# Kernel tuning notes

Measured on AMD Instinct MI355X. Metric: run time of the kernel, lower is better.

Reference implementation:

```python
import jax, jax.numpy as jnp
import numpy as np

VOCAB = 32000
EMBED = 256
HIDDEN = 512
BATCH = 64
SEQ = 512


def setup_inputs() -> dict:
    key = jax.random.key(0)
    k1, k2, k3, k4, k5, k6 = jax.random.split(key, 6)
    s = 1.0 / np.sqrt(HIDDEN)
    return {
        "source": jax.random.randint(k1, (BATCH, SEQ), 0, VOCAB),
        "embedding": jax.random.normal(k2, (VOCAB, EMBED), dtype=jnp.float32),
        "W_ih": jax.random.uniform(k3, (EMBED, HIDDEN), dtype=jnp.float32, minval=-s, maxval=s),
        "W_hh": jax.random.uniform(k4, (HIDDEN, HIDDEN), dtype=jnp.float32, minval=-s, maxval=s),
        "b_ih": jax.random.uniform(k5, (HIDDEN,), dtype=jnp.float32, minval=-s, maxval=s),
        "b_hh": jax.random.uniform(k6, (HIDDEN,), dtype=jnp.float32, minval=-s, maxval=s),
    }


def reference(source, embedding, W_ih, W_hh, b_ih, b_hh):
    # Embedding lookup: (B, S, E)
    embedded = embedding[source]
    batch_size = source.shape[0]
    h0 = jnp.zeros((batch_size, HIDDEN), dtype=embedding.dtype)

    def step(h, x_t):
        # Elman RNN cell: h' = tanh(x W_ih + b_ih + h W_hh + b_hh)
        h_new = jnp.tanh(x_t @ W_ih + b_ih + h @ W_hh + b_hh)
        return h_new, h_new

    # scan over time axis: xs shape (S, B, E)
    _, hiddens = jax.lax.scan(step, h0, jnp.swapaxes(embedded, 0, 1))
    # hiddens: (S, B, H) -> (B, S, H)
    return jnp.swapaxes(hiddens, 0, 1)
```

## Files before the change

### kernel.cpp

```cpp
#include <hip/hip_runtime.h>
#include <stdint.h>

#define EMBED  256
#define HIDDEN 512
#define BATCH  64
#define SEQ    512

typedef _Float16 f16x8 __attribute__((ext_vector_type(8)));
typedef _Float16 f16x4 __attribute__((ext_vector_type(4)));
typedef float    f32x4 __attribute__((ext_vector_type(4)));


#define WIH_FRAGS (8 * 32 * 64 * 8)
#define WHH_FRAGS (16 * 32 * 64 * 8)

__global__ void prep_pack(const float* __restrict__ W_ih,
                          const float* __restrict__ W_hh,
                          unsigned short* __restrict__ wih_p,
                          unsigned short* __restrict__ whh_p) {
    int tid = blockIdx.x * blockDim.x + threadIdx.x;
    if (tid < WIH_FRAGS) {
        int j = tid & 7, l = (tid >> 3) & 63, nt = (tid >> 9) & 31, s = tid >> 14;
        int k   = s * 32 + ((l >> 4) << 3) + j;
        int col = (nt << 4) + (l & 15);
        wih_p[tid] = __builtin_bit_cast(unsigned short, (_Float16)W_ih[k * HIDDEN + col]);
    } else {
        int t2 = tid - WIH_FRAGS;
        if (t2 < WHH_FRAGS) {
            int j = t2 & 7, l = (t2 >> 3) & 63, mt = (t2 >> 9) & 31, s = t2 >> 14;
            int k   = s * 32 + ((l >> 4) << 3) + j;
            int col = (mt << 4) + (l & 15);
            whh_p[t2] = __builtin_bit_cast(unsigned short, (_Float16)W_hh[k * HIDDEN + col]);
        }
    }
}

__global__ __launch_bounds__(256) void enc_gemm_ih(
    const int* __restrict__ source,
    const float* __restrict__ embedding,
    const unsigned short* __restrict__ wih_p,
    const float* __restrict__ b_ih,
    const float* __restrict__ b_hh,
    float* __restrict__ out)
{
    const int lane = threadIdx.x & 63;
    const int mt   = (blockIdx.x << 2) + (threadIdx.x >> 6);
    const int r0   = mt << 4;
    const int g    = lane >> 4;
    const int c    = lane & 15;

    const int idx = source[r0 + c];
    const float* erow = embedding + (size_t)idx * EMBED;

    f16x8 afrag[8];
#pragma unroll
    for (int s = 0; s < 8; ++s) {
        const float* p = erow + (s << 5) + (g << 3);
        f32x4 f0 = *(const f32x4*)p;
        f32x4 f1 = *(const f32x4*)(p + 4);
        f16x8 a;
        a[0] = (_Float16)f0[0]; a[1] = (_Float16)f0[1];
        a[2] = (_Float16)f0[2]; a[3] = (_Float16)f0[3];
        a[4] = (_Float16)f1[0]; a[5] = (_Float16)f1[1];
        a[6] = (_Float16)f1[2]; a[7] = (_Float16)f1[3];
        afrag[s] = a;
    }

    const f16x8* wp = (const f16x8*)wih_p;
    for (int nt = 0; nt < 32; ++nt) {
        f32x4 acc = {0.f, 0.f, 0.f, 0.f};
#pragma unroll
        for (int s = 0; s < 8; ++s) {
            f16x8 bfr = wp[(((s << 5) + nt) << 6) + lane];
            acc = __builtin_amdgcn_mfma_f32_16x16x32_f16(afrag[s], bfr, acc, 0, 0, 0);
        }
        const int col  = (nt << 4) + c;
        const float bias = b_ih[col] + b_hh[col];
        char* ob = (char*)out + (size_t)(r0 + (g << 2)) * 2048 + 1024 + (col << 1);
#pragma unroll
        for (int r = 0; r < 4; ++r)
            *(_Float16*)(ob + (size_t)r * 2048) = (_Float16)(acc[r] + bias);
    }
}

__global__ __launch_bounds__(512, 1) void enc_rnn(
    const unsigned short* __restrict__ whh_p,
    float* __restrict__ out)
{
    extern __shared__ char lds[];
    char* hbase = lds;
    char* wbase = lds + 32768;

    const int tid  = threadIdx.x;
    const int lane = tid & 63;
    const int w    = tid >> 6;
    const int g    = lane >> 4;
    const int c    = lane & 15;
    const int cx   = c & 7;
    const int mt0  = w << 2;

    const f16x8* wp = (const f16x8*)whh_p;

    {
        char* wl0 = wbase + ((w * 12) << 10) + (lane << 4);
#pragma unroll
        for (int fid = 0; fid < 12; ++fid) {
            int s = 9 + (fid >> 2), m = fid & 3;
            *(f16x8*)(wl0 + (fid << 10)) = wp[((s * 32 + mt0 + m) << 6) + lane];
        }
    }
    for (int i = tid; i < 32768 / 4; i += 512) ((int*)hbase)[i] = 0;

    f16x8 wreg[36];
#pragma unroll
    for (int s = 0; s < 9; ++s)
#pragma unroll
        for (int m = 0; m < 4; ++m)
            wreg[s * 4 + m] = wp[((s * 32 + mt0 + m) << 6) + lane];
#pragma unroll
    for (int i = 0; i < 36; ++i)
        asm volatile("" : "+v"(wreg[i]));

    __syncthreads();

    const int ch = cx >> 2;
    char* hb2 = hbase + (c << 10) + ((g ^ (cx & 3)) << 4);
    char* hev = hb2 + (ch << 6);
    char* hod = hb2 - (ch << 6);
    char* hw[4];
#pragma unroll
    for (int m = 0; m < 4; ++m) {
        int u = (w << 3) | ((m ^ (cx >> 1)) << 1) | ((g >> 1) ^ (cx & 1));
        hw[m] = hbase + (c << 10) + (u << 4) + ((g & 1) << 3);
    }
    char* ga = (char*)out + (size_t)((blockIdx.x << 4) + c) * SEQ * 2048
             + (w << 7) + (g << 3);
    const char* sp12 = (const char*)whh_p + ((12 * 32 + mt0) << 10) + (lane << 4);
    const char* sp13 = (const char*)whh_p + ((13 * 32 + mt0) << 10) + (lane << 4);
    const char* sp14 = (const char*)whh_p + ((14 * 32 + mt0) << 10) + (lane << 4);
    const char* sp15 = (const char*)whh_p + ((15 * 32 + mt0) << 10) + (lane << 4);
    char* wl = wbase + ((w * 12) << 10) + (lane << 4);

    auto STEP = [&](int RB, int RBN, int TB) {
        f16x8 sA[4], sB[4], sC[4];
#pragma unroll
        for (int m = 0; m < 4; ++m) sA[m] = *(const f16x8*)(sp12 + (m << 10));
#pragma unroll
        for (int m = 0; m < 4; ++m) sB[m] = *(const f16x8*)(sp13 + (m << 10));
        f16x4 pre[4];
#pragma unroll
        for (int m = 0; m < 4; ++m)
            pre[m] = *(const f16x4*)(ga + TB + 1024 + (m << 5));

        f32x4 acc[4];
#pragma unroll
        for (int m = 0; m < 4; ++m) acc[m] = (f32x4){0.f, 0.f, 0.f, 0.f};

#pragma unroll
        for (int s = 0; s < 16; ++s) {
            f16x8 h = *(const f16x8*)(((s & 1) ? hod : hev) + (s << 6) + RB);
            if (s == 6) {
#pragma unroll
                for (int m = 0; m < 4; ++m) sC[m] = *(const f16x8*)(sp14 + (m << 10));
            }
#pragma unroll
            for (int m = 0; m < 4; ++m) {
                f16x8 wv;
                if (s < 9)        wv = wreg[s * 4 + m];
                else if (s < 12)  wv = *(const f16x8*)(wl + ((((s - 9) << 2) | m) << 10));
                else if (s == 12) wv = sA[m];
                else if (s == 13) wv = sB[m];
                else if (s == 14) wv = sC[m];
                else              wv = sA[m];
                acc[m] = __builtin_amdgcn_mfma_f32_16x16x32_f16(wv, h, acc[m], 0, 0, 0);
            }
            if (s == 12) {
#pragma unroll
                for (int m = 0; m < 4; ++m) sA[m] = *(const f16x8*)(sp15 + (m << 10));
            }
        }

#pragma unroll
        for (int m = 0; m < 4; ++m) {
            f16x4 hv;
#pragma unroll
            for (int r = 0; r < 4; ++r) {
                float x  = acc[m][r] + (float)pre[m][r];
                float e  = __expf(2.0f * x);
                hv[r] = (_Float16)(1.0f - 2.0f * __builtin_amdgcn_rcpf(e + 1.0f));
            }
            *(f16x4*)(ga + TB + (m << 5)) = hv;
            *(f16x4*)(hw[m] + RBN) = hv;
        }
        __syncthreads();
    };

#pragma unroll 1
    for (int tp = 0; tp < SEQ; tp += 2) {
        STEP(0, 16384, 0);
        STEP(16384, 0, 2048);
        ga += 4096;
    }
}

__global__ __launch_bounds__(256) void expand_rows(float* __restrict__ out) {
    const int lane = threadIdx.x & 63;
    const int row  = (blockIdx.x << 2) + (threadIdx.x >> 6);
    char* rp = (char*)out + ((size_t)row << 11);
    f16x8 v = *(const f16x8*)(rp + (lane << 4));
    f32x4 lo, hi;
#pragma unroll
    for (int i = 0; i < 4; ++i) { lo[i] = (float)v[i]; hi[i] = (float)v[i + 4]; }
    *(f32x4*)(rp + (lane << 5))      = lo;
    *(f32x4*)(rp + (lane << 5) + 16) = hi;
}

extern "C" void kernel_launch(void* const* d_in, const int* in_sizes, int n_in,
                              void* d_out, int out_size, void* d_ws, size_t ws_size,
                              hipStream_t stream) {
    const int*   source    = (const int*)d_in[0];
    const float* embedding = (const float*)d_in[1];
    const float* W_ih      = (const float*)d_in[2];
    const float* W_hh      = (const float*)d_in[3];
    const float* b_ih      = (const float*)d_in[4];
    const float* b_hh      = (const float*)d_in[5];
    float* out = (float*)d_out;

    unsigned short* wih_p = (unsigned short*)d_ws;
    unsigned short* whh_p = wih_p + WIH_FRAGS;

    prep_pack<<<(WIH_FRAGS + WHH_FRAGS) / 256, 256, 0, stream>>>(W_ih, W_hh, wih_p, whh_p);
    enc_gemm_ih<<<512, 256, 0, stream>>>(source, embedding, wih_p, b_ih, b_hh, out);
    enc_rnn<<<4, 512, 131072, stream>>>(whh_p, out);
    expand_rows<<<8192, 256, 0, stream>>>(out);
}
```

Before: 1.299 ms.

## Hold 11 W_hh k-slices in registers via inline-asm MFMA chain in RNN step

Grows the register-resident part of W_hh from 9 to 11 k-slices. The first 11 MFMA groups are issued from one inline-asm block so the compiler cannot spill or reorder those weight registers. LDS-staged slices shift to 11-13, and only slices 14-15 are still streamed from global memory each step, down from four. Register pressure goes up sharply with 44 f16x8 weight registers plus 11 h fragments, and the min-blocks hint in launch_bounds is dropped, so spills or lost latency hiding are possible.

```diff
diff --git a/kernel.cpp b/kernel.cpp
--- a/kernel.cpp
+++ b/kernel.cpp
@@ -83,7 +83,15 @@
     }
 }
 
-__global__ __launch_bounds__(512, 1) void enc_rnn(
+#define MM(s) \
+  "v_mfma_f32_16x16x32_f16 %[a0], %[w" #s "0], %[h" #s "], %[a0]\n\t" \
+  "v_mfma_f32_16x16x32_f16 %[a1], %[w" #s "1], %[h" #s "], %[a1]\n\t" \
+  "v_mfma_f32_16x16x32_f16 %[a2], %[w" #s "2], %[h" #s "], %[a2]\n\t" \
+  "v_mfma_f32_16x16x32_f16 %[a3], %[w" #s "3], %[h" #s "], %[a3]\n\t"
+#define WOPS(s) [w##s##0]"v"(wv[4*s+0]), [w##s##1]"v"(wv[4*s+1]), \
+                [w##s##2]"v"(wv[4*s+2]), [w##s##3]"v"(wv[4*s+3])
+
+__global__ __launch_bounds__(512) void enc_rnn(
     const unsigned short* __restrict__ whh_p,
     float* __restrict__ out)
 {
@@ -105,21 +113,16 @@
         char* wl0 = wbase + ((w * 12) << 10) + (lane << 4);
 #pragma unroll
         for (int fid = 0; fid < 12; ++fid) {
-            int s = 9 + (fid >> 2), m = fid & 3;
+            int s = 11 + (fid >> 2), m = fid & 3;
             *(f16x8*)(wl0 + (fid << 10)) = wp[((s * 32 + mt0 + m) << 6) + lane];
         }
     }
     for (int i = tid; i < 32768 / 4; i += 512) ((int*)hbase)[i] = 0;
 
-    f16x8 wreg[36];
-#pragma unroll
-    for (int s = 0; s < 9; ++s)
-#pragma unroll
-        for (int m = 0; m < 4; ++m)
-            wreg[s * 4 + m] = wp[((s * 32 + mt0 + m) << 6) + lane];
-#pragma unroll
-    for (int i = 0; i < 36; ++i)
-        asm volatile("" : "+v"(wreg[i]));
+    f16x8 wv[44];
+#pragma unroll
+    for (int f = 0; f < 44; ++f)
+        wv[f] = wp[(((f >> 2) * 32 + mt0 + (f & 3)) << 6) + lane];
 
     __syncthreads();
 
@@ -135,49 +138,60 @@
     }
     char* ga = (char*)out + (size_t)((blockIdx.x << 4) + c) * SEQ * 2048
              + (w << 7) + (g << 3);
-    const char* sp12 = (const char*)whh_p + ((12 * 32 + mt0) << 10) + (lane << 4);
-    const char* sp13 = (const char*)whh_p + ((13 * 32 + mt0) << 10) + (lane << 4);
     const char* sp14 = (const char*)whh_p + ((14 * 32 + mt0) << 10) + (lane << 4);
     const char* sp15 = (const char*)whh_p + ((15 * 32 + mt0) << 10) + (lane << 4);
     char* wl = wbase + ((w * 12) << 10) + (lane << 4);
 
     auto STEP = [&](int RB, int RBN, int TB) {
-        f16x8 sA[4], sB[4], sC[4];
-#pragma unroll
-        for (int m = 0; m < 4; ++m) sA[m] = *(const f16x8*)(sp12 + (m << 10));
-#pragma unroll
-        for (int m = 0; m < 4; ++m) sB[m] = *(const f16x8*)(sp13 + (m << 10));
+        f16x8 hh[11];
+#pragma unroll
+        for (int s = 0; s < 11; ++s)
+            hh[s] = *(const f16x8*)(((s & 1) ? hod : hev) + (s << 6) + RB);
+
+        f32x4 a0 = {0.f,0.f,0.f,0.f}, a1 = {0.f,0.f,0.f,0.f};
+        f32x4 a2 = {0.f,0.f,0.f,0.f}, a3 = {0.f,0.f,0.f,0.f};
+        asm volatile(
+            MM(0) MM(1) MM(2) MM(3) MM(4) MM(5) MM(6) MM(7) MM(8) MM(9) MM(10)
+            : [a0]"+v"(a0), [a1]"+v"(a1), [a2]"+v"(a2), [a3]"+v"(a3)
+            : WOPS(0), WOPS(1), WOPS(2), WOPS(3), WOPS(4), WOPS(5), WOPS(6),
+              WOPS(7), WOPS(8), WOPS(9), WOPS(10),
+              [h0]"v"(hh[0]), [h1]"v"(hh[1]), [h2]"v"(hh[2]), [h3]"v"(hh[3]),
+              [h4]"v"(hh[4]), [h5]"v"(hh[5]), [h6]"v"(hh[6]), [h7]"v"(hh[7]),
+              [h8]"v"(hh[8]), [h9]"v"(hh[9]), [h10]"v"(hh[10])
+            : "memory");
+
+        f16x8 sA[4], sB[4];
+#pragma unroll
+        for (int m = 0; m < 4; ++m) sA[m] = *(const f16x8*)(sp14 + (m << 10));
+#pragma unroll
+        for (int m = 0; m < 4; ++m) sB[m] = *(const f16x8*)(sp15 + (m << 10));
         f16x4 pre[4];
 #pragma unroll
         for (int m = 0; m < 4; ++m)
             pre[m] = *(const f16x4*)(ga + TB + 1024 + (m << 5));
 
-        f32x4 acc[4];
-#pragma unroll
-        for (int m = 0; m < 4; ++m) acc[m] = (f32x4){0.f, 0.f, 0.f, 0.f};
-
-#pragma unroll
-        for (int s = 0; s < 16; ++s) {
+        f32x4 acc[4] = {a0, a1, a2, a3};
+
+#pragma unroll
+        for (int s = 11; s < 14; ++s) {
             f16x8 h = *(const f16x8*)(((s & 1) ? hod : hev) + (s << 6) + RB);
-            if (s == 6) {
-#pragma unroll
-                for (int m = 0; m < 4; ++m) sC[m] = *(const f16x8*)(sp14 + (m << 10));
+#pragma unroll
+            for (int m = 0; m < 4; ++m) {
+                f16x8 wvv = *(const f16x8*)(wl + ((((s - 11) << 2) | m) << 10));
+                acc[m] = __builtin_amdgcn_mfma_f32_16x16x32_f16(wvv, h, acc[m], 0, 0, 0);
             }
-#pragma unroll
-            for (int m = 0; m < 4; ++m) {
-                f16x8 wv;
-                if (s < 9)        wv = wreg[s * 4 + m];
-                else if (s < 12)  wv = *(const f16x8*)(wl + ((((s - 9) << 2) | m) << 10));
-                else if (s == 12) wv = sA[m];
-                else if (s == 13) wv = sB[m];
-                else if (s == 14) wv = sC[m];
-                else              wv = sA[m];
-                acc[m] = __builtin_amdgcn_mfma_f32_16x16x32_f16(wv, h, acc[m], 0, 0, 0);
-            }
-            if (s == 12) {
-#pragma unroll
-                for (int m = 0; m < 4; ++m) sA[m] = *(const f16x8*)(sp15 + (m << 10));
-            }
+        }
+        {
+            f16x8 h = *(const f16x8*)(hev + (14 << 6) + RB);
+#pragma unroll
+            for (int m = 0; m < 4; ++m)
+                acc[m] = __builtin_amdgcn_mfma_f32_16x16x32_f16(sA[m], h, acc[m], 0, 0, 0);
+        }
+        {
+            f16x8 h = *(const f16x8*)(hod + (15 << 6) + RB);
+#pragma unroll
+            for (int m = 0; m < 4; ++m)
+                acc[m] = __builtin_amdgcn_mfma_f32_16x16x32_f16(sB[m], h, acc[m], 0, 0, 0);
         }
 
 #pragma unroll
```

New measurement: 1.438 ms. 1.11x slower.
